# Optimization experiments

Hardware: AMD Instinct MI355X
Metric: run time of the kernel (lower is better)

The kernel has to match this reference:

```python
import jax, jax.numpy as jnp
import numpy as np

LEAKY_SLOPE = 0.2  # PyG GATv2Conv default negative_slope


def gatv2_layer(x, src, dst, Wl, Wr, att, bias, concat):
    """PyG GATv2Conv (eval mode, dropout off, self-loops already in src/dst).
    x: [N, Din]; Wl/Wr: [Din, H*C]; att: [H, C]; bias: [H*C] or [C].
    """
    N = x.shape[0]
    H, C = att.shape
    xl = (x @ Wl).reshape(N, H, C)   # source transform
    xr = (x @ Wr).reshape(N, H, C)   # target transform
    # per-edge GATv2 score: att . leakyrelu(x_l[j] + x_r[i])
    e = jax.nn.leaky_relu(xl[src] + xr[dst], negative_slope=LEAKY_SLOPE)  # [E, H, C]
    score = jnp.einsum('ehc,hc->eh', e, att)                              # [E, H]
    # segment softmax over incoming edges of each dst node
    m = jax.ops.segment_max(score, dst, num_segments=N)                   # [N, H]
    a = jnp.exp(score - m[dst])
    denom = jax.ops.segment_sum(a, dst, num_segments=N)                   # [N, H]
    alpha = a / denom[dst]                                                # [E, H]
    out = jax.ops.segment_sum(xl[src] * alpha[..., None], dst, num_segments=N)  # [N, H, C]
    out = out.reshape(N, H * C) if concat else out.mean(axis=1)
    return out + bias


def setup_inputs() -> dict:
    key = jax.random.key(0)
    ks = jax.random.split(key, 10)
    N, D, E = 20000, 128, 320000
    HID, HEADS, OUT = 64, 8, 32
    x = jax.random.normal(ks[0], (N, D), dtype=jnp.float32)
    edge_index = jax.random.randint(ks[1], (2, E), 0, N)
    glorot = lambda k, shape, fan: jax.random.normal(k, shape, jnp.float32) * (1.0 / np.sqrt(fan))
    W1l = glorot(ks[2], (D, HEADS * HID), D)
    W1r = glorot(ks[3], (D, HEADS * HID), D)
    att1 = glorot(ks[4], (HEADS, HID), HID)
    b1 = jnp.zeros((HEADS * HID,), jnp.float32)
    W2l = glorot(ks[5], (HEADS * HID, 64), HEADS * HID)
    W2r = glorot(ks[6], (HEADS * HID, 64), HEADS * HID)
    att2 = glorot(ks[7], (1, 64), 64)
    b2 = jnp.zeros((64,), jnp.float32)
    Wlin = glorot(ks[8], (64, OUT), 64)
    blin = jnp.zeros((OUT,), jnp.float32)
    return {"x": x, "edge_index": edge_index, "W1l": W1l, "W1r": W1r, "att1": att1,
            "b1": b1, "W2l": W2l, "W2r": W2r, "att2": att2, "b2": b2,
            "Wlin": Wlin, "blin": blin}


def reference(x, edge_index, W1l, W1r, att1, b1, W2l, W2r, att2, b2, Wlin, blin):
    N = x.shape[0]
    loop = jnp.arange(N)
    src = jnp.concatenate([edge_index[0], loop])  # PyG add_self_loops=True
    dst = jnp.concatenate([edge_index[1], loop])
    h = jax.nn.elu(gatv2_layer(x, src, dst, W1l, W1r, att1, b1, concat=True))
    h = jax.nn.elu(gatv2_layer(h, src, dst, W2l, W2r, att2, b2, concat=False))
    return jax.nn.elu(h @ Wlin + blin)
```

## Files before the change

kernel.cpp:

```cpp
#include <hip/hip_runtime.h>
#include <hip/hip_bf16.h>

typedef __attribute__((ext_vector_type(8))) short short8;
typedef __attribute__((ext_vector_type(4))) short short4v;
typedef __attribute__((ext_vector_type(4))) float floatx4;
typedef __attribute__((ext_vector_type(2))) float float2v;
typedef __attribute__((ext_vector_type(4))) int int4v;
typedef __attribute__((ext_vector_type(2))) int int2v;

#define LOG2E 1.44269504f

__device__ __forceinline__ short f2b(float f) {
    __hip_bfloat16 hb = __float2bfloat16(f);
    unsigned short us; __builtin_memcpy(&us, &hb, 2);
    return (short)us;
}
__device__ __forceinline__ float2v bpair(int p) {
    unsigned ulo = ((unsigned)p) << 16;
    unsigned uhi = ((unsigned)p) & 0xFFFF0000u;
    float flo, fhi;
    __builtin_memcpy(&flo, &ulo, 4);
    __builtin_memcpy(&fhi, &uhi, 4);
    float2v r; r.x = flo; r.y = fhi; return r;
}

__device__ __forceinline__ float2v pk_add(float2v a, float2v b) {
    float2v d;
    asm("v_pk_add_f32 %0, %1, %2" : "=v"(d) : "v"(a), "v"(b));
    return d;
}
__device__ __forceinline__ float2v pk_fma(float2v a, float2v b, float2v c) {
    float2v d;
    asm("v_pk_fma_f32 %0, %1, %2, %3" : "=v"(d) : "v"(a), "v"(b), "v"(c));
    return d;
}
__device__ __forceinline__ float2v pk_abs(float2v a) {
    float2v d;
    d.x = __builtin_fabsf(a.x);
    d.y = __builtin_fabsf(a.y);
    return d;
}

template<int CTRL>
__device__ __forceinline__ float dppadd(float x) {
    int xi; __builtin_memcpy(&xi, &x, 4);
    int yi = __builtin_amdgcn_update_dpp(0, xi, CTRL, 0xF, 0xF, false);
    float y; __builtin_memcpy(&y, &yi, 4);
    return x + y;
}
__device__ __forceinline__ float red8(float x) {
    x = dppadd<0xB1>(x);
    x = dppadd<0x4E>(x);
    x = dppadd<0x141>(x);
    return x;
}
__device__ __forceinline__ float red16(float x) {
    return dppadd<0x140>(red8(x));
}

__global__ void prep_all(const float* __restrict__ W1l, const float* __restrict__ W1r,
                         const float* __restrict__ W2l, const float* __restrict__ W2r,
                         short* __restrict__ w1t, short* __restrict__ w2t,
                         const int* __restrict__ esrc, const int* __restrict__ edst,
                         int E, int N, int* __restrict__ counts,
                         unsigned short* __restrict__ srcs) {
    int tid = blockIdx.x * blockDim.x + threadIdx.x;
    int ET = E + N;
    if (tid < ET) {
        int d, s;
        if (tid < E) { d = edst[tid]; s = esrc[tid]; }
        else { d = tid - E; s = d; }
        int pos = atomicAdd(&counts[d], 1);
        if (pos < 64) srcs[(d << 6) + pos] = (unsigned short)s;
    }
    int idx = tid;
    if (idx < 131072) {
        int n = idx >> 7, k = idx & 127;
        float v = (n < 512) ? W1l[k * 512 + n] : W1r[k * 512 + (n - 512)];
        w1t[idx] = f2b(v);
        return;
    }
    idx -= 131072;
    if (idx < 65536) {
        int n = idx >> 9, k = idx & 511;
        float v = (n < 64) ? W2l[k * 64 + n] : W2r[k * 64 + (n - 64)];
        w2t[idx] = f2b(v);
    }
}

__global__ void bin_count(const int* __restrict__ counts, int* __restrict__ bincnt,
                          int N) {
    __shared__ int lcnt[65];
    int t = threadIdx.x;
    if (t < 65) lcnt[t] = 0;
    __syncthreads();
    int i = blockIdx.x * blockDim.x + t;
    if (i < N) { int d = counts[i]; d = d > 64 ? 64 : d; atomicAdd(&lcnt[d], 1); }
    __syncthreads();
    if (t < 65 && lcnt[t] > 0) atomicAdd(&bincnt[t], lcnt[t]);
}
__global__ void bin_prefix(const int* __restrict__ bincnt, int* __restrict__ binoff) {
    if (threadIdx.x == 0) {
        int s = 0;
        for (int b = 0; b <= 64; ++b) { binoff[b] = s; s += bincnt[b]; }
    }
}
__global__ void bin_scatter(const int* __restrict__ counts, int* __restrict__ binoff,
                            int* __restrict__ perm, int N) {
    __shared__ int lcnt[65];
    __shared__ int lbase[65];
    int t = threadIdx.x;
    if (t < 65) lcnt[t] = 0;
    __syncthreads();
    int i = blockIdx.x * blockDim.x + t;
    int d = 0, lpos = 0;
    bool v = i < N;
    if (v) { d = counts[i]; d = d > 64 ? 64 : d; lpos = atomicAdd(&lcnt[d], 1); }
    __syncthreads();
    if (t < 65 && lcnt[t] > 0) lbase[t] = atomicAdd(&binoff[t], lcnt[t]);
    __syncthreads();
    if (v) perm[lbase[d] + lpos] = i;
}

__global__ __launch_bounds__(256) void gemm1(const float* __restrict__ A,
                                             const short* __restrict__ Bt,
                                             short* __restrict__ xl1, short* __restrict__ xr1,
                                             int M) {
    __shared__ short As[64 * 136];
    __shared__ short Bs[128 * 136];
    int t = threadIdx.x;
    int w = t >> 6, L = t & 63, q = L >> 4, s = L & 15;
    int p = blockIdx.x + (blockIdx.y << 3);
    int my = gridDim.y;
    int ww = (p & 7) * my + (p >> 3);
    int M0 = (ww >> 3) * 64, N0 = (ww & 7) * 128;
    #pragma unroll
    for (int i = 0; i < 8; ++i) {
        int c = t + i * 256;
        int r = c >> 5, col4 = c & 31;
        int gr = M0 + r;
        floatx4 v = {};
        if (gr < M) v = *(const floatx4*)(A + (size_t)gr * 128 + col4 * 4);
        short4v o; o[0] = f2b(v[0]); o[1] = f2b(v[1]); o[2] = f2b(v[2]); o[3] = f2b(v[3]);
        *(short4v*)(&As[r * 136 + col4 * 4]) = o;
    }
    #pragma unroll
    for (int i = 0; i < 8; ++i) {
        int c = t + i * 256;
        int r = c >> 4, col = (c & 15) * 8;
        short8 v = *(const short8*)(Bt + (size_t)(N0 + r) * 128 + col);
        *(short8*)(&Bs[r * 136 + col]) = v;
    }
    __syncthreads();
    short8 a[4];
    #pragma unroll
    for (int kk = 0; kk < 4; ++kk)
        a[kk] = *(const short8*)(&As[(w * 16 + s) * 136 + kk * 32 + q * 8]);
    floatx4 acc[8] = {};
    #pragma unroll
    for (int tt = 0; tt < 8; ++tt) {
        #pragma unroll
        for (int kk = 0; kk < 4; ++kk) {
            short8 b = *(const short8*)(&Bs[(tt * 16 + s) * 136 + kk * 32 + q * 8]);
            acc[tt] = __builtin_amdgcn_mfma_f32_16x16x32_bf16(a[kk], b, acc[tt], 0, 0, 0);
        }
    }
    __syncthreads();
    #pragma unroll
    for (int tt = 0; tt < 8; ++tt) {
        #pragma unroll
        for (int rg = 0; rg < 4; ++rg) {
            int rl = w * 16 + q * 4 + rg;
            As[rl * 136 + tt * 16 + s] = f2b(acc[tt][rg]);
        }
    }
    __syncthreads();
    short* Cb = (N0 < 512) ? xl1 : xr1;
    int cb = (N0 < 512) ? N0 : N0 - 512;
    size_t M64 = (size_t)M * 64;
    #pragma unroll
    for (int i = 0; i < 4; ++i) {
        int c = t + i * 256;
        int r = c >> 4, col = (c & 15) * 8;
        int row = M0 + r;
        if (row < M) {
            short8 v = *(const short8*)(&As[r * 136 + col]);
            int cc = cb + col;
            *(short8*)(Cb + (size_t)(cc >> 6) * M64 + (size_t)row * 64 + (cc & 63)) = v;
        }
    }
}

__global__ __launch_bounds__(256) void gemm2(const short* __restrict__ A,
                                             const short* __restrict__ Bt,
                                             short* __restrict__ C, int M) {
    __shared__ short As[32 * 72];
    __shared__ short Bs[64 * 72];
    int t = threadIdx.x;
    int w = t >> 6, L = t & 63, q = L >> 4, s = L & 15;
    int rw = (w >> 1) * 16, cw = (w & 1) * 32;
    int p = blockIdx.x + gridDim.x * blockIdx.y;
    int nwg = gridDim.x * 2;
    int qq = nwg >> 3, rr = nwg & 7;
    int kx = p & 7, tx = p >> 3;
    int ww = (kx < rr ? kx * (qq + 1) : rr * (qq + 1) + (kx - rr) * qq) + tx;
    int M0 = (ww >> 1) * 32, N0 = (ww & 1) * 64;
    size_t M64 = (size_t)M * 64;
    floatx4 acc[2] = {};
    for (int k0 = 0; k0 < 512; k0 += 64) {
        {
            int r = t >> 3, col = (t & 7) * 8;
            int gr = M0 + r;
            short8 v = {};
            if (gr < M) v = *(const short8*)(A + (size_t)(k0 >> 6) * M64 + (size_t)gr * 64 + col);
            *(short8*)(&As[r * 72 + col]) = v;
        }
        #pragma unroll
        for (int i = 0; i < 2; ++i) {
            int c = t + i * 256;
            int r = c >> 3, col = (c & 7) * 8;
            short8 v = *(const short8*)(Bt + (size_t)(N0 + r) * 512 + k0 + col);
            *(short8*)(&Bs[r * 72 + col]) = v;
        }
        __syncthreads();
        #pragma unroll
        for (int kk = 0; kk < 2; ++kk) {
            short8 a = *(const short8*)(&As[(rw + s) * 72 + kk * 32 + q * 8]);
            #pragma unroll
            for (int tt = 0; tt < 2; ++tt) {
                short8 b = *(const short8*)(&Bs[(cw + tt * 16 + s) * 72 + kk * 32 + q * 8]);
                acc[tt] = __builtin_amdgcn_mfma_f32_16x16x32_bf16(a, b, acc[tt], 0, 0, 0);
            }
        }
        __syncthreads();
    }
    #pragma unroll
    for (int tt = 0; tt < 2; ++tt) {
        #pragma unroll
        for (int rg = 0; rg < 4; ++rg) {
            int rl = rw + q * 4 + rg;
            As[rl * 72 + cw + tt * 16 + s] = f2b(acc[tt][rg]);
        }
    }
    __syncthreads();
    {
        int r = t >> 3, col = (t & 7) * 8;
        int row = M0 + r;
        if (row < M) {
            short8 v = *(const short8*)(&As[r * 72 + col]);
            *(short8*)(C + (size_t)row * 128 + N0 + col) = v;
        }
    }
}

__global__ __launch_bounds__(256) void gat_l1(const short* __restrict__ xlh,
                       const short* __restrict__ xrh,
                       const int* __restrict__ counts,
                       const unsigned short* __restrict__ srcs,
                       const int* __restrict__ perm,
                       const float* __restrict__ att, const float* __restrict__ bias,
                       short* __restrict__ h1h, int Nn) {
    int bid = blockIdx.x;
    int h = bid & 7, nb = bid >> 3;
    int t = threadIdx.x;
    int w = t >> 6, L = t & 63;
    int u = L >> 3;
    int c = L & 7;
    int o8 = c * 8;
    int idx = (nb * 4 + w) * 8 + u;
    bool inode = idx < Nn;
    int ic = perm[inode ? idx : 0];
    size_t slice = (size_t)h * ((size_t)Nn * 64);
    const char* Bp = (const char*)(xlh + slice);
    int co = c << 4;

    float2v xrv[4], at6[4], at4[4];
    {
        float av[8];
        *(floatx4*)av       = *(const floatx4*)(att + h * 64 + o8);
        *(floatx4*)(av + 4) = *(const floatx4*)(att + h * 64 + o8 + 4);
        int4v x4 = *(const int4v*)(xrh + slice + (size_t)ic * 64 + o8);
        #pragma unroll
        for (int k = 0; k < 4; ++k) {
            xrv[k] = bpair(x4[k]);
            at6[k].x = av[2 * k]     * (0.6f * LOG2E);
            at6[k].y = av[2 * k + 1] * (0.6f * LOG2E);
            at4[k].x = av[2 * k]     * (0.4f * LOG2E);
            at4[k].y = av[2 * k + 1] * (0.4f * LOG2E);
        }
    }
    int deg = counts[ic]; deg = deg > 64 ? 64 : deg;
    if (!inode) deg = 0;
    int degw = deg;
    degw = max(degw, __shfl_xor(degw, 8, 64));
    degw = max(degw, __shfl_xor(degw, 16, 64));
    degw = max(degw, __shfl_xor(degw, 32, 64));

    const unsigned short* sp = srcs + ((size_t)ic << 6);
    int4v J = *(const int4v*)(sp + c * 8);
    int ubase = L & 56;

    float2v acc[4] = {};
    float dnm = 0.f;

    for (int ow = 0; ow < 8; ++ow) {
        int s0 = ow << 3;
        if (s0 >= degw) break;
        int lane = ubase + ow;
        int j01 = __shfl(J[0], lane, 64);
        int j23 = __shfl(J[1], lane, 64);
        int j45 = __shfl(J[2], lane, 64);
        int j67 = __shfl(J[3], lane, 64);
        int js[8];
        js[0] = j01 & 0x7FFF; js[1] = (j01 >> 16) & 0x7FFF;
        js[2] = j23 & 0x7FFF; js[3] = (j23 >> 16) & 0x7FFF;
        js[4] = j45 & 0x7FFF; js[5] = (j45 >> 16) & 0x7FFF;
        js[6] = j67 & 0x7FFF; js[7] = (j67 >> 16) & 0x7FFF;
        int4v rows[8];
        #pragma unroll
        for (int k = 0; k < 8; ++k)
            rows[k] = *(const int4v*)(Bp + (((unsigned)js[k] << 7) + co));
        #pragma unroll
        for (int k = 0; k < 8; ++k) {
            float2v v[4]; float2v pp = {};
            #pragma unroll
            for (int q = 0; q < 4; ++q) {
                v[q] = bpair(rows[k][q]);
                float2v tv = pk_add(v[q], xrv[q]);
                pp = pk_fma(at6[q], tv, pp);
                pp = pk_fma(at4[q], pk_abs(tv), pp);
            }
            float e2 = __builtin_amdgcn_exp2f(red8(pp.x + pp.y));
            e2 = (s0 + k < deg) ? e2 : 0.f;
            dnm += e2;
            float2v ev; ev.x = e2; ev.y = e2;
            #pragma unroll
            for (int q = 0; q < 4; ++q)
                acc[q] = pk_fma(ev, v[q], acc[q]);
        }
    }

    if (inode) {
        float inv = 1.f / dnm;
        float bv[8];
        *(floatx4*)bv       = *(const floatx4*)(bias + h * 64 + o8);
        *(floatx4*)(bv + 4) = *(const floatx4*)(bias + h * 64 + o8 + 4);
        short8 ov;
        #pragma unroll
        for (int k = 0; k < 4; ++k) {
            float ox = fmaf(acc[k].x, inv, bv[2 * k]);
            float oy = fmaf(acc[k].y, inv, bv[2 * k + 1]);
            ox = ox > 0.f ? ox : __expf(ox) - 1.f;
            oy = oy > 0.f ? oy : __expf(oy) - 1.f;
            ov[2 * k] = f2b(ox);
            ov[2 * k + 1] = f2b(oy);
        }
        *(short8*)(h1h + slice + (size_t)ic * 64 + o8) = ov;
    }
}

__global__ __launch_bounds__(256) void gat_l2_fin(const short* __restrict__ x2,
                        const int* __restrict__ counts,
                        const unsigned short* __restrict__ srcs,
                        const float* __restrict__ att, const float* __restrict__ bias,
                        const float* __restrict__ Wlin, const float* __restrict__ blin,
                        float* __restrict__ out, int Nn) {
    __shared__ float Ws[2048];
    __shared__ float bs[32];
    __shared__ float h2s[4][64];
    int t = threadIdx.x;
    for (int idx = t; idx < 2048; idx += 256) Ws[idx] = Wlin[idx];
    if (t < 32) bs[t] = blin[t];
    __syncthreads();
    int w = t >> 6, L = t & 63;
    int i = blockIdx.x * 4 + w;
    if (i >= Nn) return;
    int g = L >> 4;
    int lc = L & 15;
    int c4 = lc * 4;
    float2v xrv[2], at6[2], at4[2];
    {
        int2v xv = *(const int2v*)(x2 + (i << 7) + 64 + c4);
        xrv[0] = bpair(xv.x);
        xrv[1] = bpair(xv.y);
        floatx4 a4 = *(const floatx4*)(att + c4);
        at6[0].x = a4[0] * (0.6f * LOG2E); at6[0].y = a4[1] * (0.6f * LOG2E);
        at6[1].x = a4[2] * (0.6f * LOG2E); at6[1].y = a4[3] * (0.6f * LOG2E);
        at4[0].x = a4[0] * (0.4f * LOG2E); at4[0].y = a4[1] * (0.4f * LOG2E);
        at4[1].x = a4[2] * (0.4f * LOG2E); at4[1].y = a4[3] * (0.4f * LOG2E);
    }
    float dnm = 0.f;
    float2v acc0 = {}, acc1 = {};
    int kb = i << 6;
    int deg = counts[i]; deg = deg > 64 ? 64 : deg;
    int ke = kb + deg;
    const int2v* x2i = (const int2v*)x2;

    auto doedge = [&](int2v Vv, bool val) {
        float2v v0 = bpair(Vv.x), v1 = bpair(Vv.y);
        float2v t0 = pk_add(v0, xrv[0]), t1 = pk_add(v1, xrv[1]);
        float2v pp = pk_fma(at6[0], t0, at4[0] * pk_abs(t0));
        pp = pk_fma(at6[1], t1, pp);
        pp = pk_fma(at4[1], pk_abs(t1), pp);
        float e = val ? __builtin_amdgcn_exp2f(red16(pp.x + pp.y)) : 0.f;
        dnm += e;
        float2v e2; e2.x = e; e2.y = e;
        acc0 = pk_fma(e2, v0, acc0);
        acc1 = pk_fma(e2, v1, acc1);
    };

    for (int k0 = kb; k0 < ke; k0 += 16) {
        int ka = k0 + g, kc = k0 + 4 + g, kd = k0 + 8 + g, kf = k0 + 12 + g;
        bool va = ka < ke, vb = kc < ke, vc = kd < ke, vd = kf < ke;
        int ja = srcs[va ? ka : kb];
        int jb = srcs[vb ? kc : kb];
        int jc = srcs[vc ? kd : kb];
        int jd = srcs[vd ? kf : kb];
        int2v Va = x2i[(ja << 5) + lc];
        int2v Vb = x2i[(jb << 5) + lc];
        int2v Vc = x2i[(jc << 5) + lc];
        int2v Vd = x2i[(jd << 5) + lc];
        doedge(Va, va);
        doedge(Vb, vb);
        doedge(Vc, vc);
        doedge(Vd, vd);
    }
    #pragma unroll
    for (int m = 16; m <= 32; m <<= 1) {
        dnm += __shfl_xor(dnm, m, 64);
        acc0.x += __shfl_xor(acc0.x, m, 64);
        acc0.y += __shfl_xor(acc0.y, m, 64);
        acc1.x += __shfl_xor(acc1.x, m, 64);
        acc1.y += __shfl_xor(acc1.y, m, 64);
    }
    float inv = 1.f / dnm;
    floatx4 bv = *(const floatx4*)(bias + c4);
    float o0 = fmaf(acc0.x, inv, bv[0]);
    float o1 = fmaf(acc0.y, inv, bv[1]);
    float o2 = fmaf(acc1.x, inv, bv[2]);
    float o3 = fmaf(acc1.y, inv, bv[3]);
    o0 = o0 > 0.f ? o0 : __expf(o0) - 1.f;
    o1 = o1 > 0.f ? o1 : __expf(o1) - 1.f;
    o2 = o2 > 0.f ? o2 : __expf(o2) - 1.f;
    o3 = o3 > 0.f ? o3 : __expf(o3) - 1.f;
    if (L < 16) {
        floatx4 hv; hv[0] = o0; hv[1] = o1; hv[2] = o2; hv[3] = o3;
        *(floatx4*)(&h2s[w][c4]) = hv;
    }
    int oc = L & 31;
    float accl = 0.f;
    #pragma unroll
    for (int kk = 0; kk < 16; ++kk) {
        floatx4 hvv = *(const floatx4*)(&h2s[w][kk * 4]);
        accl = fmaf(hvv[0], Ws[(kk * 4 + 0) * 32 + oc], accl);
        accl = fmaf(hvv[1], Ws[(kk * 4 + 1) * 32 + oc], accl);
        accl = fmaf(hvv[2], Ws[(kk * 4 + 2) * 32 + oc], accl);
        accl = fmaf(hvv[3], Ws[(kk * 4 + 3) * 32 + oc], accl);
    }
    if (L < 32) {
        float r = accl + bs[oc];
        r = r > 0.f ? r : __expf(r) - 1.f;
        out[(size_t)i * 32 + oc] = r;
    }
}

extern "C" void kernel_launch(void* const* d_in, const int* in_sizes, int n_in,
                              void* d_out, int out_size, void* d_ws, size_t ws_size,
                              hipStream_t stream) {
    const float* x    = (const float*)d_in[0];
    const int*   ei   = (const int*)d_in[1];
    const float* W1l  = (const float*)d_in[2];
    const float* W1r  = (const float*)d_in[3];
    const float* att1 = (const float*)d_in[4];
    const float* b1   = (const float*)d_in[5];
    const float* W2l  = (const float*)d_in[6];
    const float* W2r  = (const float*)d_in[7];
    const float* att2 = (const float*)d_in[8];
    const float* b2   = (const float*)d_in[9];
    const float* Wlin = (const float*)d_in[10];
    const float* blin = (const float*)d_in[11];

    const int N  = in_sizes[0] / 128;
    const int E  = in_sizes[1] / 2;

    char* w = (char*)d_ws;
    size_t cur = 0;
    auto take = [&](size_t bytes) -> void* {
        void* p = w + cur;
        cur = (cur + bytes + 255) & ~(size_t)255;
        return p;
    };
    int*            counts = (int*)take((size_t)N * 4);
    unsigned short* srcs   = (unsigned short*)take((size_t)N * 64 * 2);
    int*   bincnt = (int*)take(65 * 4);
    int*   binoff = (int*)take(65 * 4);
    int*   perm   = (int*)take((size_t)N * 4);
    short* w1t    = (short*)take((size_t)1024 * 128 * 2);
    short* w2t    = (short*)take((size_t)128 * 512 * 2);
    short* xl1    = (short*)take((size_t)N * 512 * 2);
    short* xr1    = (short*)take((size_t)N * 512 * 2);
    short* h1     = (short*)take((size_t)N * 512 * 2);
    short* x2     = (short*)take((size_t)N * 128 * 2);

    hipMemsetAsync(counts, 0, (size_t)N * 4, stream);
    hipMemsetAsync(bincnt, 0, 65 * 4, stream);
    int nprep = (E + N) > 196608 ? (E + N) : 196608;
    prep_all<<<(nprep + 255) / 256, 256, 0, stream>>>(W1l, W1r, W2l, W2r, w1t, w2t,
                                                      ei, ei + E, E, N, counts, srcs);

    bin_count<<<(N + 255) / 256, 256, 0, stream>>>(counts, bincnt, N);
    bin_prefix<<<1, 64, 0, stream>>>(bincnt, binoff);
    bin_scatter<<<(N + 255) / 256, 256, 0, stream>>>(counts, binoff, perm, N);

    gemm1<<<dim3(8, (N + 63) / 64), 256, 0, stream>>>(x, w1t, xl1, xr1, N);
    gat_l1<<<8 * ((N + 31) / 32), 256, 0, stream>>>(xl1, xr1, counts, srcs, perm,
                                                    att1, b1, h1, N);

    gemm2<<<dim3((N + 31) / 32, 2), 256, 0, stream>>>(h1, w2t, x2, N);
    gat_l2_fin<<<(N + 3) / 4, 256, 0, stream>>>(x2, counts, srcs, att2, b2, Wlin, blin,
                                                (float*)d_out, N);
}
```

Baseline: 205.7 us.

## Pre-convert x to bf16 in prep kernel, reverse degree order, zero srcs

Moves the fp32-to-bf16 conversion of x out of gemm1 into prep_all. gemm1 no longer repeats that conversion in each of the 8 column-tile blocks; it reads half-size bf16 rows instead. It also reverses the degree-sorted permutation so high-degree nodes are scheduled first, and zero-fills srcs before use. The source-index unpack now uses the full 16-bit value rather than masking to 15 bits. The cost is an extra intermediate buffer, a write and read of it, and a memset of srcs.

```diff
diff --git a/kernel.cpp b/kernel.cpp
--- a/kernel.cpp
+++ b/kernel.cpp
@@ -58,9 +58,11 @@
     return dppadd<0x140>(red8(x));
 }
 
-__global__ void prep_all(const float* __restrict__ W1l, const float* __restrict__ W1r,
+__global__ void prep_all(const float* __restrict__ x,
+                         const float* __restrict__ W1l, const float* __restrict__ W1r,
                          const float* __restrict__ W2l, const float* __restrict__ W2r,
-                         short* __restrict__ w1t, short* __restrict__ w2t,
+                         short* __restrict__ xb, short* __restrict__ w1t,
+                         short* __restrict__ w2t, int nx4,
                          const int* __restrict__ esrc, const int* __restrict__ edst,
                          int E, int N, int* __restrict__ counts,
                          unsigned short* __restrict__ srcs) {
@@ -74,6 +76,13 @@
         if (pos < 64) srcs[(d << 6) + pos] = (unsigned short)s;
     }
     int idx = tid;
+    if (idx < nx4) {
+        floatx4 v = *(const floatx4*)(x + idx * 4);
+        short4v o; o[0] = f2b(v[0]); o[1] = f2b(v[1]); o[2] = f2b(v[2]); o[3] = f2b(v[3]);
+        *(short4v*)(xb + idx * 4) = o;
+        return;
+    }
+    idx -= nx4;
     if (idx < 131072) {
         int n = idx >> 7, k = idx & 127;
         float v = (n < 512) ? W1l[k * 512 + n] : W1r[k * 512 + (n - 512)];
@@ -119,10 +128,10 @@
     __syncthreads();
     if (t < 65 && lcnt[t] > 0) lbase[t] = atomicAdd(&binoff[t], lcnt[t]);
     __syncthreads();
-    if (v) perm[lbase[d] + lpos] = i;
-}
-
-__global__ __launch_bounds__(256) void gemm1(const float* __restrict__ A,
+    if (v) perm[N - 1 - (lbase[d] + lpos)] = i;
+}
+
+__global__ __launch_bounds__(256) void gemm1(const short* __restrict__ A,
                                              const short* __restrict__ Bt,
                                              short* __restrict__ xl1, short* __restrict__ xr1,
                                              int M) {
@@ -135,14 +144,13 @@
     int ww = (p & 7) * my + (p >> 3);
     int M0 = (ww >> 3) * 64, N0 = (ww & 7) * 128;
     #pragma unroll
-    for (int i = 0; i < 8; ++i) {
+    for (int i = 0; i < 4; ++i) {
         int c = t + i * 256;
-        int r = c >> 5, col4 = c & 31;
+        int r = c >> 4, col = (c & 15) * 8;
         int gr = M0 + r;
-        floatx4 v = {};
-        if (gr < M) v = *(const floatx4*)(A + (size_t)gr * 128 + col4 * 4);
-        short4v o; o[0] = f2b(v[0]); o[1] = f2b(v[1]); o[2] = f2b(v[2]); o[3] = f2b(v[3]);
-        *(short4v*)(&As[r * 136 + col4 * 4]) = o;
+        short8 v = {};
+        if (gr < M) v = *(const short8*)(A + (size_t)gr * 128 + col);
+        *(short8*)(&As[r * 136 + col]) = v;
     }
     #pragma unroll
     for (int i = 0; i < 8; ++i) {
@@ -312,10 +320,10 @@
         int j45 = __shfl(J[2], lane, 64);
         int j67 = __shfl(J[3], lane, 64);
         int js[8];
-        js[0] = j01 & 0x7FFF; js[1] = (j01 >> 16) & 0x7FFF;
-        js[2] = j23 & 0x7FFF; js[3] = (j23 >> 16) & 0x7FFF;
-        js[4] = j45 & 0x7FFF; js[5] = (j45 >> 16) & 0x7FFF;
-        js[6] = j67 & 0x7FFF; js[7] = (j67 >> 16) & 0x7FFF;
+        js[0] = j01 & 0xFFFF; js[1] = ((unsigned)j01) >> 16;
+        js[2] = j23 & 0xFFFF; js[3] = ((unsigned)j23) >> 16;
+        js[4] = j45 & 0xFFFF; js[5] = ((unsigned)j45) >> 16;
+        js[6] = j67 & 0xFFFF; js[7] = ((unsigned)j67) >> 16;
         int4v rows[8];
         #pragma unroll
         for (int k = 0; k < 8; ++k)
@@ -495,6 +503,7 @@
     int*   bincnt = (int*)take(65 * 4);
     int*   binoff = (int*)take(65 * 4);
     int*   perm   = (int*)take((size_t)N * 4);
+    short* xb     = (short*)take((size_t)N * 128 * 2);
     short* w1t    = (short*)take((size_t)1024 * 128 * 2);
     short* w2t    = (short*)take((size_t)128 * 512 * 2);
     short* xl1    = (short*)take((size_t)N * 512 * 2);
@@ -503,16 +512,19 @@
     short* x2     = (short*)take((size_t)N * 128 * 2);
 
     hipMemsetAsync(counts, 0, (size_t)N * 4, stream);
+    hipMemsetAsync(srcs, 0, (size_t)N * 64 * 2, stream);
     hipMemsetAsync(bincnt, 0, 65 * 4, stream);
-    int nprep = (E + N) > 196608 ? (E + N) : 196608;
-    prep_all<<<(nprep + 255) / 256, 256, 0, stream>>>(W1l, W1r, W2l, W2r, w1t, w2t,
-                                                      ei, ei + E, E, N, counts, srcs);
+    int nx4 = N * 32;
+    int nconv = nx4 + 131072 + 65536;
+    int nprep = (E + N) > nconv ? (E + N) : nconv;
+    prep_all<<<(nprep + 255) / 256, 256, 0, stream>>>(x, W1l, W1r, W2l, W2r, xb, w1t, w2t,
+                                                      nx4, ei, ei + E, E, N, counts, srcs);
 
     bin_count<<<(N + 255) / 256, 256, 0, stream>>>(counts, bincnt, N);
     bin_prefix<<<1, 64, 0, stream>>>(bincnt, binoff);
     bin_scatter<<<(N + 255) / 256, 256, 0, stream>>>(counts, binoff, perm, N);
 
-    gemm1<<<dim3(8, (N + 63) / 64), 256, 0, stream>>>(x, w1t, xl1, xr1, N);
+    gemm1<<<dim3(8, (N + 63) / 64), 256, 0, stream>>>(xb, w1t, xl1, xr1, N);
     gat_l1<<<8 * ((N + 31) / 32), 256, 0, stream>>>(xl1, xr1, counts, srcs, perm,
                                                     att1, b1, h1, N);
 
```

Result: no change. 202.5 us (-1.6%).

## Fuse bin prefix into scatter, merge memsets, reverse perm order, widen final kernel

Applied to the files above, without the earlier changes.

Removes the single-thread bin_prefix kernel by having each scatter block compute the prefix over the 65 bins itself, and merges the two memsets into one by placing the bin counters right after counts. The permutation is now written in reverse, so high-degree nodes are scheduled first in layer 1. The layer-1 inner loop replaces per-lane index loads plus four shuffles with a wave-uniform vector load of 8 source indices, prefetched one octet ahead. The final layer-2 kernel moves from 256-thread to 512-thread blocks, handling 8 nodes per block and amortizing the Wlin staging into shared memory. The trade-offs are a redundant serial prefix sum in every scatter block and more register use for the prefetched indices.

```diff
diff --git a/kernel.cpp b/kernel.cpp
--- a/kernel.cpp
+++ b/kernel.cpp
@@ -99,16 +99,13 @@
     __syncthreads();
     if (t < 65 && lcnt[t] > 0) atomicAdd(&bincnt[t], lcnt[t]);
 }
-__global__ void bin_prefix(const int* __restrict__ bincnt, int* __restrict__ binoff) {
-    if (threadIdx.x == 0) {
-        int s = 0;
-        for (int b = 0; b <= 64; ++b) { binoff[b] = s; s += bincnt[b]; }
-    }
-}
-__global__ void bin_scatter(const int* __restrict__ counts, int* __restrict__ binoff,
+__global__ void bin_scatter(const int* __restrict__ counts,
+                            const int* __restrict__ bincnt,
+                            int* __restrict__ binclaim,
                             int* __restrict__ perm, int N) {
     __shared__ int lcnt[65];
     __shared__ int lbase[65];
+    __shared__ int pref[65];
     int t = threadIdx.x;
     if (t < 65) lcnt[t] = 0;
     __syncthreads();
@@ -117,9 +114,16 @@
     bool v = i < N;
     if (v) { d = counts[i]; d = d > 64 ? 64 : d; lpos = atomicAdd(&lcnt[d], 1); }
     __syncthreads();
-    if (t < 65 && lcnt[t] > 0) lbase[t] = atomicAdd(&binoff[t], lcnt[t]);
-    __syncthreads();
-    if (v) perm[lbase[d] + lpos] = i;
+    if (t == 0) {
+        int s = 0;
+        #pragma unroll 1
+        for (int b = 0; b <= 64; ++b) { pref[b] = s; s += bincnt[b]; }
+    }
+    __syncthreads();
+    if (t < 65 && lcnt[t] > 0)
+        lbase[t] = pref[t] + atomicAdd(&binclaim[t], lcnt[t]);
+    __syncthreads();
+    if (v) perm[N - 1 - (lbase[d] + lpos)] = i;
 }
 
 __global__ __launch_bounds__(256) void gemm1(const float* __restrict__ A,
@@ -297,25 +301,21 @@
     degw = max(degw, __shfl_xor(degw, 32, 64));
 
     const unsigned short* sp = srcs + ((size_t)ic << 6);
-    int4v J = *(const int4v*)(sp + c * 8);
-    int ubase = L & 56;
 
     float2v acc[4] = {};
     float dnm = 0.f;
 
+    int4v Jw = *(const int4v*)sp;
     for (int ow = 0; ow < 8; ++ow) {
         int s0 = ow << 3;
         if (s0 >= degw) break;
-        int lane = ubase + ow;
-        int j01 = __shfl(J[0], lane, 64);
-        int j23 = __shfl(J[1], lane, 64);
-        int j45 = __shfl(J[2], lane, 64);
-        int j67 = __shfl(J[3], lane, 64);
+        int4v Jn = Jw;
+        if (s0 + 8 < degw) Jn = *(const int4v*)(sp + s0 + 8);
         int js[8];
-        js[0] = j01 & 0x7FFF; js[1] = (j01 >> 16) & 0x7FFF;
-        js[2] = j23 & 0x7FFF; js[3] = (j23 >> 16) & 0x7FFF;
-        js[4] = j45 & 0x7FFF; js[5] = (j45 >> 16) & 0x7FFF;
-        js[6] = j67 & 0x7FFF; js[7] = (j67 >> 16) & 0x7FFF;
+        js[0] = Jw[0] & 0x7FFF; js[1] = (Jw[0] >> 16) & 0x7FFF;
+        js[2] = Jw[1] & 0x7FFF; js[3] = (Jw[1] >> 16) & 0x7FFF;
+        js[4] = Jw[2] & 0x7FFF; js[5] = (Jw[2] >> 16) & 0x7FFF;
+        js[6] = Jw[3] & 0x7FFF; js[7] = (Jw[3] >> 16) & 0x7FFF;
         int4v rows[8];
         #pragma unroll
         for (int k = 0; k < 8; ++k)
@@ -338,6 +338,7 @@
             for (int q = 0; q < 4; ++q)
                 acc[q] = pk_fma(ev, v[q], acc[q]);
         }
+        Jw = Jn;
     }
 
     if (inode) {
@@ -359,7 +360,7 @@
     }
 }
 
-__global__ __launch_bounds__(256) void gat_l2_fin(const short* __restrict__ x2,
+__global__ __launch_bounds__(512) void gat_l2_fin(const short* __restrict__ x2,
                         const int* __restrict__ counts,
                         const unsigned short* __restrict__ srcs,
                         const float* __restrict__ att, const float* __restrict__ bias,
@@ -367,13 +368,13 @@
                         float* __restrict__ out, int Nn) {
     __shared__ float Ws[2048];
     __shared__ float bs[32];
-    __shared__ float h2s[4][64];
+    __shared__ float h2s[8][64];
     int t = threadIdx.x;
-    for (int idx = t; idx < 2048; idx += 256) Ws[idx] = Wlin[idx];
+    for (int idx = t; idx < 2048; idx += 512) Ws[idx] = Wlin[idx];
     if (t < 32) bs[t] = blin[t];
     __syncthreads();
     int w = t >> 6, L = t & 63;
-    int i = blockIdx.x * 4 + w;
+    int i = blockIdx.x * 8 + w;
     if (i >= Nn) return;
     int g = L >> 4;
     int lc = L & 15;
@@ -490,10 +491,10 @@
         cur = (cur + bytes + 255) & ~(size_t)255;
         return p;
     };
-    int*            counts = (int*)take((size_t)N * 4);
-    unsigned short* srcs   = (unsigned short*)take((size_t)N * 64 * 2);
-    int*   bincnt = (int*)take(65 * 4);
-    int*   binoff = (int*)take(65 * 4);
+    int* counts = (int*)take(((size_t)N + 130) * 4);
+    int* bincnt   = counts + N;
+    int* binclaim = counts + N + 65;
+    unsigned short* srcs = (unsigned short*)take((size_t)N * 64 * 2);
     int*   perm   = (int*)take((size_t)N * 4);
     short* w1t    = (short*)take((size_t)1024 * 128 * 2);
     short* w2t    = (short*)take((size_t)128 * 512 * 2);
@@ -502,21 +503,19 @@
     short* h1     = (short*)take((size_t)N * 512 * 2);
     short* x2     = (short*)take((size_t)N * 128 * 2);
 
-    hipMemsetAsync(counts, 0, (size_t)N * 4, stream);
-    hipMemsetAsync(bincnt, 0, 65 * 4, stream);
+    hipMemsetAsync(counts, 0, ((size_t)N + 130) * 4, stream);
     int nprep = (E + N) > 196608 ? (E + N) : 196608;
     prep_all<<<(nprep + 255) / 256, 256, 0, stream>>>(W1l, W1r, W2l, W2r, w1t, w2t,
                                                       ei, ei + E, E, N, counts, srcs);
 
     bin_count<<<(N + 255) / 256, 256, 0, stream>>>(counts, bincnt, N);
-    bin_prefix<<<1, 64, 0, stream>>>(bincnt, binoff);
-    bin_scatter<<<(N + 255) / 256, 256, 0, stream>>>(counts, binoff, perm, N);
+    bin_scatter<<<(N + 255) / 256, 256, 0, stream>>>(counts, bincnt, binclaim, perm, N);
 
     gemm1<<<dim3(8, (N + 63) / 64), 256, 0, stream>>>(x, w1t, xl1, xr1, N);
     gat_l1<<<8 * ((N + 31) / 32), 256, 0, stream>>>(xl1, xr1, counts, srcs, perm,
                                                     att1, b1, h1, N);
 
     gemm2<<<dim3((N + 31) / 32, 2), 256, 0, stream>>>(h1, w2t, x2, N);
-    gat_l2_fin<<<(N + 3) / 4, 256, 0, stream>>>(x2, counts, srcs, att2, b2, Wlin, blin,
+    gat_l2_fin<<<(N + 7) / 8, 512, 0, stream>>>(x2, counts, srcs, att2, b2, Wlin, blin,
                                                 (float*)d_out, N);
 }
```

Measured after the change: 200.7 us. 2.4% less time.
